# Performance work log

Measured on AMD Instinct MI355X. Metric: run time of the kernel, lower is better.

Reference implementation:

```python
import jax, jax.numpy as jnp
import numpy as np
import math

THETA = 10000.0

def _rope(x, pos):
    # x: [B, H, S, Dh], pos: [S]
    d = x.shape[-1]
    inv_freq = 1.0 / (THETA ** (jnp.arange(0, d, 2, dtype=jnp.float32) / d))  # [Dh/2]
    ang = pos.astype(jnp.float32)[:, None] * inv_freq[None, :]                # [S, Dh/2]
    cos, sin = jnp.cos(ang), jnp.sin(ang)
    x1, x2 = x[..., 0::2], x[..., 1::2]
    r1 = x1 * cos - x2 * sin
    r2 = x1 * sin + x2 * cos
    return jnp.stack([r1, r2], axis=-1).reshape(x.shape)

def setup_inputs() -> dict:
    key = jax.random.key(0)
    ks = jax.random.split(key, 5)
    B, S, D = 2, 1024, 2048
    Dkv = 512
    scale = 1.0 / math.sqrt(D)
    return {
        "X": jax.random.normal(ks[0], (B, S, D), dtype=jnp.float32),
        "token_positions": jnp.arange(S, dtype=jnp.int32),
        "q_w": jax.random.normal(ks[1], (D, D), dtype=jnp.float32) * scale,
        "k_w": jax.random.normal(ks[2], (Dkv, D), dtype=jnp.float32) * scale,
        "v_w": jax.random.normal(ks[3], (Dkv, D), dtype=jnp.float32) * scale,
        "o_w": jax.random.normal(ks[4], (D, D), dtype=jnp.float32) * scale,
    }

def reference(X, token_positions, q_w, k_w, v_w, o_w):
    B, S, D = X.shape
    H, Hkv = 32, 8
    Dh = D // H
    G = H // Hkv  # query heads per KV head

    Q = (X @ q_w.T).reshape(B, S, H, Dh).transpose(0, 2, 1, 3)      # [B,H,S,Dh]
    K = (X @ k_w.T).reshape(B, S, Hkv, Dh).transpose(0, 2, 1, 3)    # [B,Hkv,S,Dh]
    V = (X @ v_w.T).reshape(B, S, Hkv, Dh).transpose(0, 2, 1, 3)    # [B,Hkv,S,Dh]

    Q = _rope(Q, token_positions)
    K = _rope(K, token_positions)

    # group query heads: [B, Hkv, G, S, Dh]
    Qg = Q.reshape(B, Hkv, G, S, Dh)
    scores = jnp.einsum('bkgqd,bkld->bkgql', Qg, K) / math.sqrt(Dh)  # [B,Hkv,G,S,S]
    causal = jnp.tril(jnp.ones((S, S), dtype=bool))
    scores = jnp.where(causal, scores, -jnp.inf)
    probs = jax.nn.softmax(scores, axis=-1)
    attn = jnp.einsum('bkgql,bkld->bkgqd', probs, V)                 # [B,Hkv,G,S,Dh]

    attn = attn.reshape(B, H, S, Dh).transpose(0, 2, 1, 3).reshape(B, S, D)
    return attn @ o_w.T
```

## Files before the change

kernel.cpp:

```cpp
#include <hip/hip_runtime.h>

typedef _Float16 f16;
typedef _Float16 half8 __attribute__((ext_vector_type(8), may_alias));
typedef _Float16 half4 __attribute__((ext_vector_type(4), may_alias));
typedef float f32x4 __attribute__((ext_vector_type(4), may_alias));

#define ROPE_KF -0.41524101186092027f

__device__ __forceinline__ void gload_lds16(const f16* g, f16* lds) {
  __builtin_amdgcn_global_load_lds(
      (const __attribute__((address_space(1))) void*)g,
      (__attribute__((address_space(3))) void*)lds, 16, 0, 0);
}

template <int N>
__device__ __forceinline__ void vm_wait() {
  if constexpr (N == 0) asm volatile("s_waitcnt vmcnt(0)" ::: "memory");
  else if constexpr (N == 3) asm volatile("s_waitcnt vmcnt(3)" ::: "memory");
  else if constexpr (N == 4) asm volatile("s_waitcnt vmcnt(4)" ::: "memory");
  else if constexpr (N == 6) asm volatile("s_waitcnt vmcnt(6)" ::: "memory");
  else if constexpr (N == 8) asm volatile("s_waitcnt vmcnt(8)" ::: "memory");
}

__device__ __forceinline__ half8 rope8(half8 v, float posf, int i0, float scale) {
  half8 r;
#pragma unroll
  for (int p = 0; p < 4; ++p) {
    const float ang = posf * exp2f(ROPE_KF * (float)(i0 + p));
    float s, c;
    sincosf(ang, &s, &c);
    const float x1 = (float)v[2 * p], x2 = (float)v[2 * p + 1];
    r[2 * p]     = (f16)((x1 * c - x2 * s) * scale);
    r[2 * p + 1] = (f16)((x1 * s + x2 * c) * scale);
  }
  return r;
}

__global__ __launch_bounds__(256) void cvt_all(const float* __restrict__ s0, f16* __restrict__ d0, int n0,
                                               const float* __restrict__ s1, f16* __restrict__ d1, int n1,
                                               const float* __restrict__ s2, f16* __restrict__ d2, int n2,
                                               const float* __restrict__ s3, f16* __restrict__ d3, int n3,
                                               const float* __restrict__ s4, f16* __restrict__ d4, int n4) {
  const int step = gridDim.x * blockDim.x * 4;
  const int base = (blockIdx.x * blockDim.x + threadIdx.x) * 4;
  auto go = [&](const float* s, f16* d, int n) {
    for (int i = base; i < n; i += step) {
      float4 v = *(const float4*)(s + i);
      half4 h;
      h[0] = (f16)v.x; h[1] = (f16)v.y; h[2] = (f16)v.z; h[3] = (f16)v.w;
      *(half4*)(d + i) = h;
    }
  };
  go(s0, d0, n0); go(s1, d1, n1); go(s2, d2, n2); go(s3, d3, n3); go(s4, d4, n4);
}

template <int OUT_F32, int BM>
__global__ __launch_bounds__(256, 2) void gemm_bt(const f16* __restrict__ A,
                                                  const f16* __restrict__ B,
                                                  void* __restrict__ Cv,
                                                  int M, int N, int K) {
  constexpr int NJ = (BM == 128) ? 4 : 2;
  constexpr int ACH = BM / 64;
  constexpr int LPS = ACH + 2;

  __shared__ alignas(16) f16 As[4][BM][32];
  __shared__ alignas(16) f16 Bs[4][128][32];
  const int tid = threadIdx.x;
  const int w = tid >> 6, l = tid & 63;
  const int m0 = blockIdx.y * BM, n0 = blockIdx.x << 7;
  const int fr = l & 15;
  const int fkz = (((l >> 4) ^ ((fr >> 1) & 3)) << 3);
  const int wr = (BM == 128) ? ((w >> 1) << 6) : 0;
  const int wc = (BM == 128) ? ((w & 1) << 6) : (w << 5);
  const int srow = l >> 2;
  const int scol = (((l & 3) ^ ((l >> 3) & 3)) << 3);

  const f16* ga = A + (size_t)(m0 + srow) * K + scol;
  const f16* gb = B + (size_t)(n0 + srow) * K + scol;

  auto stage = [&](int t) {
    const int buf = t & 3, k0 = t << 5;
#pragma unroll
    for (int c = 0; c < ACH; ++c) {
      const int rb = (w * ACH + c) << 4;
      gload_lds16(ga + (size_t)rb * K + k0, &As[buf][rb][0]);
    }
#pragma unroll
    for (int c = 0; c < 2; ++c) {
      const int rb = (w * 2 + c) << 4;
      gload_lds16(gb + (size_t)rb * K + k0, &Bs[buf][rb][0]);
    }
  };

  f32x4 acc[4][NJ] = {};

  const int nk = K >> 5;
  stage(0); stage(1); stage(2);
  for (int t = 0; t < nk; ++t) {
    if (t + 2 < nk) vm_wait<2 * LPS>();
    else if (t + 1 < nk) vm_wait<LPS>();
    else vm_wait<0>();
    __builtin_amdgcn_s_barrier();
    __builtin_amdgcn_sched_barrier(0);
    if (t + 3 < nk) stage(t + 3);
    const int buf = t & 3;
    half8 af[4], bf[NJ];
#pragma unroll
    for (int i = 0; i < 4; ++i) af[i] = *(const half8*)&As[buf][wr + i * 16 + fr][fkz];
#pragma unroll
    for (int j = 0; j < NJ; ++j) bf[j] = *(const half8*)&Bs[buf][wc + j * 16 + fr][fkz];
    __builtin_amdgcn_s_setprio(1);
#pragma unroll
    for (int i = 0; i < 4; ++i)
#pragma unroll
      for (int j = 0; j < NJ; ++j)
        acc[i][j] = __builtin_amdgcn_mfma_f32_16x16x32_f16(af[i], bf[j], acc[i][j], 0, 0, 0);
    __builtin_amdgcn_s_setprio(0);
    __builtin_amdgcn_sched_barrier(0);
  }

  const int orow = (l >> 4) << 2;
#pragma unroll
  for (int i = 0; i < 4; ++i) {
#pragma unroll
    for (int j = 0; j < NJ; ++j) {
      const int col = n0 + wc + j * 16 + fr;
#pragma unroll
      for (int r = 0; r < 4; ++r) {
        const size_t idx = (size_t)(m0 + wr + i * 16 + orow + r) * N + col;
        if (OUT_F32) ((float*)Cv)[idx] = acc[i][j][r];
        else ((f16*)Cv)[idx] = (f16)acc[i][j][r];
      }
    }
  }
}

__global__ __launch_bounds__(256) void repack_kv(const f16* __restrict__ QKV,
                                                 const int* __restrict__ pos,
                                                 f16* __restrict__ Kp,
                                                 f16* __restrict__ Vt) {
  const int kt = blockIdx.x, kvh = blockIdx.y, b = blockIdx.z;
  const int tid = threadIdx.x;
  __shared__ f16 vs[64][72];
  const size_t tile = ((size_t)((b * 8 + kvh) * 16 + kt)) * 4096;
  const f16* kbase = QKV + 2048 + kvh * 64;
  const f16* vbase = QKV + 2560 + kvh * 64;
#pragma unroll
  for (int p = 0; p < 2; ++p) {
    const int c = tid + p * 256;
    const int row = c >> 3, slot = c & 7;
    const size_t grow = (size_t)(b * 1024 + kt * 64 + row) * 3072;
    half8 kk = *(const half8*)(kbase + grow + slot * 8);
    kk = rope8(kk, (float)pos[kt * 64 + row], slot << 2, 1.0f);
    *(half8*)(Kp + tile + row * 64 + ((slot ^ (row & 7)) << 3)) = kk;
    *(half8*)&vs[row][slot * 8] = *(const half8*)(vbase + grow + slot * 8);
  }
  __syncthreads();
#pragma unroll
  for (int p = 0; p < 2; ++p) {
    const int c = tid + p * 256;
    const int d = c >> 3, oct = c & 7;
    half8 vv;
#pragma unroll
    for (int m = 0; m < 8; ++m) vv[m] = vs[oct * 8 + m][d];
    *(half8*)(Vt + tile + d * 64 + ((oct ^ (d & 7)) << 3)) = vv;
  }
}

__global__ __launch_bounds__(256) void attn_fwd(const f16* __restrict__ QKV,
                                                const f16* __restrict__ Kp,
                                                const f16* __restrict__ Vt,
                                                const int* __restrict__ pos,
                                                f16* __restrict__ O) {
  const int flat = blockIdx.x + (blockIdx.y << 3) + (blockIdx.z << 8);
  const int rmid = ((flat & 7) << 6) + (flat >> 3);
  const int pr = rmid & 7, h = (rmid >> 3) & 31, b = rmid >> 8;
  const int kvh = h >> 2;
  const int tid = threadIdx.x, w = tid >> 6, l = tid & 63;
  const int fr = l & 15, g = l >> 4;
  const int orow = g << 2;
  const int qtA = pr, qtB = 15 - pr;

  __shared__ alignas(16) char KsB[3][8192];
  __shared__ alignas(16) char VtB[3][8192];
  __shared__ alignas(16) f16 Ps[4][16][72];

  auto KS = [&](int buf, int row, int slot) -> f16* {
    return (f16*)(KsB[buf] + row * 128 + ((slot ^ (row & 7)) << 4));
  };
  auto VT = [&](int buf, int d, int oct) -> f16* {
    return (f16*)(VtB[buf] + d * 128 + ((oct ^ (d & 7)) << 4));
  };

  const int sA = qtA * 64 + w * 16 + fr, sB = qtB * 64 + w * 16 + fr;
  const float pA = (float)pos[sA], pB = (float)pos[sB];
  const size_t qoff = (size_t)(b * 1024 + w * 16 + fr) * 3072 + h * 64 + (g << 3);
  const f16* qA = QKV + qoff + (size_t)qtA * 64 * 3072;
  const f16* qB = QKV + qoff + (size_t)qtB * 64 * 3072;
  const half8 aA0 = rope8(*(const half8*)qA, pA, g << 2, 0.125f);
  const half8 aA1 = rope8(*(const half8*)(qA + 32), pA, 16 + (g << 2), 0.125f);
  const half8 aB0 = rope8(*(const half8*)qB, pB, g << 2, 0.125f);
  const half8 aB1 = rope8(*(const half8*)(qB + 32), pB, 16 + (g << 2), 0.125f);

  float rmA[4], rlA[4], rmB[4], rlB[4];
  f32x4 oA[4] = {}, oB[4] = {};
#pragma unroll
  for (int r = 0; r < 4; ++r) { rmA[r] = rmB[r] = -3.0e38f; rlA[r] = rlB[r] = 0.f; }

  const size_t tbase = ((size_t)((b * 8 + kvh) * 16)) * 4096;
  const f16* kp0 = Kp + tbase + w * 1024 + (l << 3);
  const f16* vp0 = Vt + tbase + w * 1024 + (l << 3);
  auto stage = [&](int kt) {
    const int buf = kt % 3;
    const f16* kp = kp0 + (size_t)kt * 4096;
    const f16* vp = vp0 + (size_t)kt * 4096;
    f16* kl = (f16*)(KsB[buf] + w * 2048);
    f16* vl = (f16*)(VtB[buf] + w * 2048);
    gload_lds16(kp, kl);
    gload_lds16(kp + 512, kl + 512);
    gload_lds16(vp, vl);
    gload_lds16(vp + 512, vl + 512);
  };

  auto compute = [&](int buf, const half8& a0, const half8& a1, float* rm, float* rl,
                     f32x4* o, int qt, int kt) {
    f32x4 s4[4] = {};
    __builtin_amdgcn_s_setprio(1);
#pragma unroll
    for (int j = 0; j < 4; ++j) {
      const half8 bk0 = *(const half8*)KS(buf, j * 16 + fr, g);
      const half8 bk1 = *(const half8*)KS(buf, j * 16 + fr, 4 + g);
      s4[j] = __builtin_amdgcn_mfma_f32_16x16x32_f16(a0, bk0, s4[j], 0, 0, 0);
      s4[j] = __builtin_amdgcn_mfma_f32_16x16x32_f16(a1, bk1, s4[j], 0, 0, 0);
    }
    __builtin_amdgcn_s_setprio(0);
    if (kt == qt) {
      const int qrow0 = qt * 64 + w * 16 + orow;
#pragma unroll
      for (int j = 0; j < 4; ++j) {
        const int col = kt * 64 + j * 16 + fr;
#pragma unroll
        for (int r = 0; r < 4; ++r)
          if (col > qrow0 + r) s4[j][r] = -1.0e30f;
      }
    }
#pragma unroll
    for (int r = 0; r < 4; ++r) {
      float mx = fmaxf(fmaxf(s4[0][r], s4[1][r]), fmaxf(s4[2][r], s4[3][r]));
#pragma unroll
      for (int off = 8; off >= 1; off >>= 1) mx = fmaxf(mx, __shfl_xor(mx, off));
      const float mn = fmaxf(rm[r], mx);
      const float sf = __expf(rm[r] - mn);
      rl[r] *= sf;
      o[0][r] *= sf; o[1][r] *= sf; o[2][r] *= sf; o[3][r] *= sf;
      rm[r] = mn;
    }
    float ps[4] = {0.f, 0.f, 0.f, 0.f};
#pragma unroll
    for (int j = 0; j < 4; ++j)
#pragma unroll
      for (int r = 0; r < 4; ++r) {
        const float p = __expf(s4[j][r] - rm[r]);
        ps[r] += p;
        Ps[w][orow + r][j * 16 + fr] = (f16)p;
      }
#pragma unroll
    for (int r = 0; r < 4; ++r) {
      float t = ps[r];
#pragma unroll
      for (int off = 8; off >= 1; off >>= 1) t += __shfl_xor(t, off);
      rl[r] += t;
    }
    __builtin_amdgcn_s_setprio(1);
#pragma unroll
    for (int kv2 = 0; kv2 < 2; ++kv2) {
      const half8 ap = *(const half8*)&Ps[w][fr][kv2 * 32 + (g << 3)];
#pragma unroll
      for (int j = 0; j < 4; ++j) {
        const half8 bv = *(const half8*)VT(buf, j * 16 + fr, kv2 * 4 + g);
        o[j] = __builtin_amdgcn_mfma_f32_16x16x32_f16(ap, bv, o[j], 0, 0, 0);
      }
    }
    __builtin_amdgcn_s_setprio(0);
  };

  stage(0);
  stage(1);
  for (int kt = 0; kt <= qtB; ++kt) {
    if (kt < qtB) vm_wait<4>();
    else vm_wait<0>();
    __builtin_amdgcn_s_barrier();
    __builtin_amdgcn_sched_barrier(0);
    if (kt + 2 <= qtB) stage(kt + 2);
    const int buf = kt % 3;
    if (kt <= qtA) compute(buf, aA0, aA1, rmA, rlA, oA, qtA, kt);
    compute(buf, aB0, aB1, rmB, rlB, oB, qtB, kt);
    __builtin_amdgcn_sched_barrier(0);
  }

#pragma unroll
  for (int j = 0; j < 4; ++j)
#pragma unroll
    for (int r = 0; r < 4; ++r) {
      const int rowA = qtA * 64 + w * 16 + orow + r;
      const int rowB = qtB * 64 + w * 16 + orow + r;
      const int col = h * 64 + j * 16 + fr;
      O[(size_t)(b * 1024 + rowA) * 2048 + col] = (f16)(oA[j][r] / rlA[r]);
      O[(size_t)(b * 1024 + rowB) * 2048 + col] = (f16)(oB[j][r] / rlB[r]);
    }
}

extern "C" void kernel_launch(void* const* d_in, const int* in_sizes, int n_in,
                              void* d_out, int out_size, void* d_ws, size_t ws_size,
                              hipStream_t stream) {
  const float* X = (const float*)d_in[0];
  const int* tokpos = (const int*)d_in[1];
  const float* qw = (const float*)d_in[2];
  const float* kw = (const float*)d_in[3];
  const float* vw = (const float*)d_in[4];
  const float* ow = (const float*)d_in[5];

  constexpr int B = 2, S = 1024, D = 2048, DKV = 512, H = 32;
  constexpr int M = B * S;
  constexpr int NQKV = D + 2 * DKV;

  char* ws = (char*)d_ws;
  f16* Xh   = (f16*)(ws);
  f16* QKVW = (f16*)(ws + (8u << 20));
  f16* owh  = (f16*)(ws + (20u << 20));
  f16* QKVc = (f16*)(ws + (28u << 20));
  f16* Ah   = (f16*)(ws + (40u << 20));
  f16* Kp   = (f16*)(ws);
  f16* Vt   = (f16*)(ws + (2u << 20));

  cvt_all<<<2048, 256, 0, stream>>>(X, Xh, M * D,
                                    qw, QKVW, D * D,
                                    kw, QKVW + (size_t)D * D, DKV * D,
                                    vw, QKVW + (size_t)(D + DKV) * D, DKV * D,
                                    ow, owh, D * D);

  gemm_bt<0, 128><<<dim3(NQKV / 128, M / 128), 256, 0, stream>>>(Xh, QKVW, QKVc, M, NQKV, D);

  repack_kv<<<dim3(16, 8, 2), 256, 0, stream>>>(QKVc, tokpos, Kp, Vt);

  attn_fwd<<<dim3(8, H, B), 256, 0, stream>>>(QKVc, Kp, Vt, tokpos, Ah);

  gemm_bt<1, 64><<<dim3(D / 128, M / 64), 256, 0, stream>>>(Ah, owh, d_out, M, D, D);
}
```

Before: 142.1 us.

## Rewrite GEMM as single-wave 64x64 tiles with register double-buffering and XCD swizzle

Replaces the 256-thread GEMM (128x128 or 64x128 tiles) with a 64-thread, single-wavefront kernel on 64x64 tiles. Each block needs no barrier, prefetches LDS fragments for the next k-step into registers while issuing MFMAs, and remaps block indices so neighbouring column tiles land on the same XCD. The goal is to remove barrier stalls and add latency hiding through many small independent blocks. The cost is lower arithmetic intensity per tile, which means more global and LDS traffic per FLOP.

```diff
diff --git a/kernel.cpp b/kernel.cpp
--- a/kernel.cpp
+++ b/kernel.cpp
@@ -16,10 +16,9 @@
 template <int N>
 __device__ __forceinline__ void vm_wait() {
   if constexpr (N == 0) asm volatile("s_waitcnt vmcnt(0)" ::: "memory");
-  else if constexpr (N == 3) asm volatile("s_waitcnt vmcnt(3)" ::: "memory");
   else if constexpr (N == 4) asm volatile("s_waitcnt vmcnt(4)" ::: "memory");
-  else if constexpr (N == 6) asm volatile("s_waitcnt vmcnt(6)" ::: "memory");
   else if constexpr (N == 8) asm volatile("s_waitcnt vmcnt(8)" ::: "memory");
+  else if constexpr (N == 16) asm volatile("s_waitcnt vmcnt(16)" ::: "memory");
 }
 
 __device__ __forceinline__ half8 rope8(half8 v, float posf, int i0, float scale) {
@@ -54,24 +53,25 @@
   go(s0, d0, n0); go(s1, d1, n1); go(s2, d2, n2); go(s3, d3, n3); go(s4, d4, n4);
 }
 
-template <int OUT_F32, int BM>
-__global__ __launch_bounds__(256, 2) void gemm_bt(const f16* __restrict__ A,
-                                                  const f16* __restrict__ B,
-                                                  void* __restrict__ Cv,
-                                                  int M, int N, int K) {
-  constexpr int NJ = (BM == 128) ? 4 : 2;
-  constexpr int ACH = BM / 64;
-  constexpr int LPS = ACH + 2;
-
-  __shared__ alignas(16) f16 As[4][BM][32];
-  __shared__ alignas(16) f16 Bs[4][128][32];
-  const int tid = threadIdx.x;
-  const int w = tid >> 6, l = tid & 63;
-  const int m0 = blockIdx.y * BM, n0 = blockIdx.x << 7;
+template <int OUT_F32>
+__global__ __launch_bounds__(64) void gemm_bt(const f16* __restrict__ A,
+                                              const f16* __restrict__ B,
+                                              void* __restrict__ Cv,
+                                              int M, int N, int K) {
+  __shared__ alignas(16) f16 As[4][64][32];
+  __shared__ alignas(16) f16 Bs[4][64][32];
+  const int l = threadIdx.x;
+
+  const int gx = gridDim.x;
+  const int chunk = gx >> 3;
+  const int flat = blockIdx.y * gx + blockIdx.x;
+  const int xcd = flat & 7, idx = flat >> 3;
+  const int bx = xcd * chunk + idx % chunk;
+  const int by = idx / chunk;
+  const int m0 = by << 6, n0 = bx << 6;
+
   const int fr = l & 15;
   const int fkz = (((l >> 4) ^ ((fr >> 1) & 3)) << 3);
-  const int wr = (BM == 128) ? ((w >> 1) << 6) : 0;
-  const int wc = (BM == 128) ? ((w & 1) << 6) : (w << 5);
   const int srow = l >> 2;
   const int scol = (((l & 3) ^ ((l >> 3) & 3)) << 3);
 
@@ -81,55 +81,72 @@
   auto stage = [&](int t) {
     const int buf = t & 3, k0 = t << 5;
 #pragma unroll
-    for (int c = 0; c < ACH; ++c) {
-      const int rb = (w * ACH + c) << 4;
-      gload_lds16(ga + (size_t)rb * K + k0, &As[buf][rb][0]);
-    }
-#pragma unroll
-    for (int c = 0; c < 2; ++c) {
-      const int rb = (w * 2 + c) << 4;
-      gload_lds16(gb + (size_t)rb * K + k0, &Bs[buf][rb][0]);
-    }
-  };
-
-  f32x4 acc[4][NJ] = {};
-
-  const int nk = K >> 5;
-  stage(0); stage(1); stage(2);
-  for (int t = 0; t < nk; ++t) {
-    if (t + 2 < nk) vm_wait<2 * LPS>();
-    else if (t + 1 < nk) vm_wait<LPS>();
-    else vm_wait<0>();
-    __builtin_amdgcn_s_barrier();
-    __builtin_amdgcn_sched_barrier(0);
-    if (t + 3 < nk) stage(t + 3);
+    for (int c = 0; c < 4; ++c) {
+      gload_lds16(ga + (size_t)(c << 4) * K + k0, &As[buf][c << 4][0]);
+      gload_lds16(gb + (size_t)(c << 4) * K + k0, &Bs[buf][c << 4][0]);
+    }
+  };
+  auto readfrags = [&](int t, half8* af, half8* bf) {
     const int buf = t & 3;
-    half8 af[4], bf[NJ];
-#pragma unroll
-    for (int i = 0; i < 4; ++i) af[i] = *(const half8*)&As[buf][wr + i * 16 + fr][fkz];
-#pragma unroll
-    for (int j = 0; j < NJ; ++j) bf[j] = *(const half8*)&Bs[buf][wc + j * 16 + fr][fkz];
+#pragma unroll
+    for (int i = 0; i < 4; ++i) {
+      af[i] = *(const half8*)&As[buf][i * 16 + fr][fkz];
+      bf[i] = *(const half8*)&Bs[buf][i * 16 + fr][fkz];
+    }
+  };
+
+  f32x4 acc[4][4] = {};
+  auto mm = [&](half8* af, half8* bf) {
     __builtin_amdgcn_s_setprio(1);
 #pragma unroll
     for (int i = 0; i < 4; ++i)
 #pragma unroll
-      for (int j = 0; j < NJ; ++j)
+      for (int j = 0; j < 4; ++j)
         acc[i][j] = __builtin_amdgcn_mfma_f32_16x16x32_f16(af[i], bf[j], acc[i][j], 0, 0, 0);
     __builtin_amdgcn_s_setprio(0);
+  };
+
+  const int nk = K >> 5;
+  half8 fa0[4], fb0[4], fa1[4], fb1[4];
+
+  stage(0); stage(1); stage(2);
+  vm_wait<16>();
+  __builtin_amdgcn_sched_barrier(0);
+  readfrags(0, fa0, fb0);
+
+  for (int t = 0; t < nk - 2; t += 2) {
+    stage(t + 3);
+    vm_wait<16>();
     __builtin_amdgcn_sched_barrier(0);
-  }
+    readfrags(t + 1, fa1, fb1);
+    mm(fa0, fb0);
+    if (t + 4 < nk) {
+      stage(t + 4);
+      vm_wait<16>();
+    } else {
+      vm_wait<8>();
+    }
+    __builtin_amdgcn_sched_barrier(0);
+    readfrags(t + 2, fa0, fb0);
+    mm(fa1, fb1);
+  }
+  vm_wait<0>();
+  __builtin_amdgcn_sched_barrier(0);
+  readfrags(nk - 1, fa1, fb1);
+  mm(fa0, fb0);
+  mm(fa1, fb1);
 
   const int orow = (l >> 4) << 2;
 #pragma unroll
   for (int i = 0; i < 4; ++i) {
 #pragma unroll
-    for (int j = 0; j < NJ; ++j) {
-      const int col = n0 + wc + j * 16 + fr;
+    for (int j = 0; j < 4; ++j) {
+      const int col = n0 + j * 16 + fr;
 #pragma unroll
       for (int r = 0; r < 4; ++r) {
-        const size_t idx = (size_t)(m0 + wr + i * 16 + orow + r) * N + col;
-        if (OUT_F32) ((float*)Cv)[idx] = acc[i][j][r];
-        else ((f16*)Cv)[idx] = (f16)acc[i][j][r];
+        const size_t cidx = (size_t)(m0 + i * 16 + orow + r) * N + col;
+        if (OUT_F32) ((float*)Cv)[cidx] = acc[i][j][r];
+        else ((f16*)Cv)[cidx] = (f16)acc[i][j][r];
       }
     }
   }
@@ -339,11 +356,11 @@
                                     vw, QKVW + (size_t)(D + DKV) * D, DKV * D,
                                     ow, owh, D * D);
 
-  gemm_bt<0, 128><<<dim3(NQKV / 128, M / 128), 256, 0, stream>>>(Xh, QKVW, QKVc, M, NQKV, D);
+  gemm_bt<0><<<dim3(NQKV / 64, M / 64), 64, 0, stream>>>(Xh, QKVW, QKVc, M, NQKV, D);
 
   repack_kv<<<dim3(16, 8, 2), 256, 0, stream>>>(QKVc, tokpos, Kp, Vt);
 
   attn_fwd<<<dim3(8, H, B), 256, 0, stream>>>(QKVc, Kp, Vt, tokpos, Ah);
 
-  gemm_bt<1, 64><<<dim3(D / 128, M / 64), 256, 0, stream>>>(Ah, owh, d_out, M, D, D);
-}
+  gemm_bt<1><<<dim3(D / 64, M / 64), 64, 0, stream>>>(Ah, owh, d_out, M, D, D);
+}
```

Measured after the change: 160.7 us. 13.1% more time.
